# Performance work log

Hardware: AMD Instinct MI355X
Metric: run time of the kernel (lower is better)

The kernel has to match this reference:

```python
import jax, jax.numpy as jnp
import numpy as np

P = 3          # spline degree
N_COEFS = 128  # number of basis functions = len(knots) - P - 1


def _basis(x, knots, p):
    """Vectorized Cox-de Boor recursion.

    x: [N] evaluation points, knots: [m]. Returns B: [m-p-1, N], the value of
    every degree-p basis function at every point. Matches the module's _B:
    k=0 -> indicator t[i] <= x < t[i+1]; equal-knot denominators contribute 0.
    """
    m = knots.shape[0]
    # degree-0 indicators: [m-1, N]
    B = ((knots[:-1, None] <= x[None, :]) & (x[None, :] < knots[1:, None])).astype(x.dtype)
    for k in range(1, p + 1):
        ld = knots[k:m - 1] - knots[:m - 1 - k]      # t[i+k]   - t[i]
        rd = knots[k + 1:m] - knots[1:m - k]         # t[i+k+1] - t[i+1]
        safe_ld = jnp.where(ld > 0, ld, 1.0)[:, None]
        safe_rd = jnp.where(rd > 0, rd, 1.0)[:, None]
        left = jnp.where(ld[:, None] > 0,
                         (x[None, :] - knots[:m - 1 - k, None]) / safe_ld, 0.0) * B[:-1]
        right = jnp.where(rd[:, None] > 0,
                          (knots[k + 1:m, None] - x[None, :]) / safe_rd, 0.0) * B[1:]
        B = left + right
    return B  # [m-p-1, N]


def setup_inputs() -> dict:
    key = jax.random.key(0)
    k1, k2, k3 = jax.random.split(key, 3)
    x = jax.random.uniform(k1, (8192,), dtype=jnp.float32)
    t = jax.random.uniform(k2, (8192,), dtype=jnp.float32)
    # open-uniform knot vector on [0,1]: p+1 repeats at each end
    interior = jnp.linspace(0.0, 1.0, N_COEFS - P + 1, dtype=jnp.float32)[1:-1]
    knots = jnp.concatenate([jnp.zeros(P + 1, jnp.float32), interior,
                             jnp.ones(P + 1, jnp.float32)])  # [N_COEFS + P + 1] = [132]
    coefs = 10.0 * jax.random.uniform(k3, (N_COEFS,), dtype=jnp.float32)
    coefs_2 = jnp.ones((N_COEFS,), jnp.float32)
    return {"x": x, "t": t, "knots": knots, "coefs": coefs, "coefs_2": coefs_2}


def reference(x, t, knots, coefs, coefs_2):
    # calculate_BSpline_2D (mode='Adam'): outer(calc_1D(x; coefs), calc_1D(t; coefs_2))
    Bx = _basis(x.ravel(), knots, P)   # [N_COEFS, Nx]
    Bt = _basis(t.ravel(), knots, P)   # [N_COEFS, Nt]
    spline_x = coefs @ Bx              # [Nx]
    spline_t = coefs_2 @ Bt            # [Nt]
    return jnp.outer(spline_x, spline_t)  # [Nx, Nt]
```

## Files before the change

### kernel.cpp

```cpp
#include <hip/hip_runtime.h>

#define NX 8192
#define NKNOTS 132
#define NCOEFS 128

__global__ void spline_eval_kernel(const float* __restrict__ x,
                                   const float* __restrict__ t,
                                   const float* __restrict__ knots,
                                   const float* __restrict__ coefs,
                                   const float* __restrict__ coefs_2,
                                   float* __restrict__ out_vals) {
    __shared__ float kn[NKNOTS];
    __shared__ float cf[2 * NCOEFS];
    if (threadIdx.x < NKNOTS) kn[threadIdx.x] = knots[threadIdx.x];
    if (threadIdx.x < NCOEFS) {
        cf[threadIdx.x] = coefs[threadIdx.x];
        cf[NCOEFS + threadIdx.x] = coefs_2[threadIdx.x];
    }
    __syncthreads();

    int gid = blockIdx.x * blockDim.x + threadIdx.x;
    if (gid >= 2 * NX) return;

    const bool is_t = (gid >= NX);
    const float v = is_t ? t[gid - NX] : x[gid];
    const float* c = is_t ? (cf + NCOEFS) : cf;

    int span = 3 + (int)(v * 125.0f);
    span = min(127, max(3, span));
    while (span > 3 && v < kn[span]) span--;
    while (span < 127 && v >= kn[span + 1]) span++;

    float N[4];
    float left[4], right[4];
    N[0] = 1.0f;
    #pragma unroll
    for (int j = 1; j <= 3; ++j) {
        left[j]  = v - kn[span + 1 - j];
        right[j] = kn[span + j] - v;
        float saved = 0.0f;
        #pragma unroll
        for (int r = 0; r < j; ++r) {
            float temp = N[r] / (right[r + 1] + left[j - r]);
            N[r] = saved + right[r + 1] * temp;
            saved = left[j - r] * temp;
        }
        N[j] = saved;
    }

    float s = 0.0f;
    #pragma unroll
    for (int r = 0; r <= 3; ++r) s += c[span - 3 + r] * N[r];

    out_vals[gid] = s;
}

__global__ void outer_kernel(const float* __restrict__ vals,
                             float4* __restrict__ out) {
    const int gid = blockIdx.x * blockDim.x + threadIdx.x;
    const int j4 = gid & 2047;
    const int i  = gid >> 11;

    const float sx = vals[i];
    const float4 st = ((const float4*)(vals + NX))[j4];

    float4 o;
    o.x = sx * st.x;
    o.y = sx * st.y;
    o.z = sx * st.z;
    o.w = sx * st.w;
    out[(size_t)i * 2048 + j4] = o;
}

extern "C" void kernel_launch(void* const* d_in, const int* in_sizes, int n_in,
                              void* d_out, int out_size, void* d_ws, size_t ws_size,
                              hipStream_t stream) {
    const float* x       = (const float*)d_in[0];
    const float* t       = (const float*)d_in[1];
    const float* knots   = (const float*)d_in[2];
    const float* coefs   = (const float*)d_in[3];
    const float* coefs_2 = (const float*)d_in[4];
    float* out = (float*)d_out;
    float* ws  = (float*)d_ws;

    spline_eval_kernel<<<(2 * NX) / 256, 256, 0, stream>>>(x, t, knots, coefs,
                                                           coefs_2, ws);

    const long long total = (long long)NX * 2048;
    outer_kernel<<<(int)(total / 256), 256, 0, stream>>>(ws, (float4*)out);
}
```

Measured before the change: 258.7 us.

## Fuse spline evaluation into tiled outer-product kernel with nontemporal stores

```diff
diff --git a/kernel.cpp b/kernel.cpp
--- a/kernel.cpp
+++ b/kernel.cpp
@@ -3,36 +3,20 @@
 #define NX 8192
 #define NKNOTS 132
 #define NCOEFS 128
+#define TILE_R 128
+#define TILE_C 256
 
-__global__ void spline_eval_kernel(const float* __restrict__ x,
-                                   const float* __restrict__ t,
-                                   const float* __restrict__ knots,
-                                   const float* __restrict__ coefs,
-                                   const float* __restrict__ coefs_2,
-                                   float* __restrict__ out_vals) {
-    __shared__ float kn[NKNOTS];
-    __shared__ float cf[2 * NCOEFS];
-    if (threadIdx.x < NKNOTS) kn[threadIdx.x] = knots[threadIdx.x];
-    if (threadIdx.x < NCOEFS) {
-        cf[threadIdx.x] = coefs[threadIdx.x];
-        cf[NCOEFS + threadIdx.x] = coefs_2[threadIdx.x];
-    }
-    __syncthreads();
+typedef float v4f __attribute__((ext_vector_type(4)));
 
-    int gid = blockIdx.x * blockDim.x + threadIdx.x;
-    if (gid >= 2 * NX) return;
-
-    const bool is_t = (gid >= NX);
-    const float v = is_t ? t[gid - NX] : x[gid];
-    const float* c = is_t ? (cf + NCOEFS) : cf;
-
+__device__ __forceinline__ float eval_spline(float v,
+                                             const float* __restrict__ kn,
+                                             const float* __restrict__ c) {
     int span = 3 + (int)(v * 125.0f);
     span = min(127, max(3, span));
     while (span > 3 && v < kn[span]) span--;
     while (span < 127 && v >= kn[span + 1]) span++;
 
-    float N[4];
-    float left[4], right[4];
+    float N[4], left[4], right[4];
     N[0] = 1.0f;
     #pragma unroll
     for (int j = 1; j <= 3; ++j) {
@@ -47,29 +31,50 @@
         }
         N[j] = saved;
     }
-
     float s = 0.0f;
     #pragma unroll
     for (int r = 0; r <= 3; ++r) s += c[span - 3 + r] * N[r];
-
-    out_vals[gid] = s;
+    return s;
 }
 
-__global__ void outer_kernel(const float* __restrict__ vals,
-                             float4* __restrict__ out) {
-    const int gid = blockIdx.x * blockDim.x + threadIdx.x;
-    const int j4 = gid & 2047;
-    const int i  = gid >> 11;
+__global__ __launch_bounds__(256) void bspline_outer_fused(
+        const float* __restrict__ x, const float* __restrict__ t,
+        const float* __restrict__ knots, const float* __restrict__ coefs,
+        const float* __restrict__ coefs_2, v4f* __restrict__ out) {
+    __shared__ float kn[NKNOTS];
+    __shared__ float cfx[NCOEFS];
+    __shared__ float cft[NCOEFS];
+    __shared__ float sx[TILE_R];
+    __shared__ float st[TILE_C];
 
-    const float sx = vals[i];
-    const float4 st = ((const float4*)(vals + NX))[j4];
+    const int tid = threadIdx.x;
+    if (tid < NKNOTS) kn[tid] = knots[tid];
+    if (tid < NCOEFS) {
+        cfx[tid] = coefs[tid];
+        cft[tid] = coefs_2[tid];
+    }
+    __syncthreads();
 
-    float4 o;
-    o.x = sx * st.x;
-    o.y = sx * st.y;
-    o.z = sx * st.z;
-    o.w = sx * st.w;
-    out[(size_t)i * 2048 + j4] = o;
+    const int row0 = blockIdx.y * TILE_R;
+    const int col0 = blockIdx.x * TILE_C;
+
+    st[tid] = eval_spline(t[col0 + tid], kn, cft);
+    if (tid < TILE_R) sx[tid] = eval_spline(x[row0 + tid], kn, cfx);
+    __syncthreads();
+
+    const int col4 = tid & 63;
+    const int r0   = tid >> 6;
+    const v4f stv = ((const v4f*)st)[col4];
+
+    size_t idx = (size_t)(row0 + r0) * (NX / 4) + (size_t)(col0 / 4) + col4;
+
+    #pragma unroll 8
+    for (int k = 0; k < TILE_R / 4; ++k) {
+        const float s = sx[r0 + 4 * k];
+        v4f o = s * stv;
+        __builtin_nontemporal_store(o, &out[idx]);
+        idx += (size_t)4 * (NX / 4);
+    }
 }
 
 extern "C" void kernel_launch(void* const* d_in, const int* in_sizes, int n_in,
@@ -80,12 +85,9 @@
     const float* knots   = (const float*)d_in[2];
     const float* coefs   = (const float*)d_in[3];
     const float* coefs_2 = (const float*)d_in[4];
-    float* out = (float*)d_out;
-    float* ws  = (float*)d_ws;
+    v4f* out = (v4f*)d_out;
 
-    spline_eval_kernel<<<(2 * NX) / 256, 256, 0, stream>>>(x, t, knots, coefs,
-                                                           coefs_2, ws);
-
-    const long long total = (long long)NX * 2048;
-    outer_kernel<<<(int)(total / 256), 256, 0, stream>>>(ws, (float4*)out);
+    dim3 grid(NX / TILE_C, NX / TILE_R);
+    bspline_outer_fused<<<grid, 256, 0, stream>>>(x, t, knots, coefs, coefs_2,
+                                                  out);
 }
```

New measurement: 271.0 us. 4.8% more time.
